# Performance work log

Measured on AMD Instinct MI355X. Metric: run time of the kernel, lower is better.

Reference implementation:

```python
import jax, jax.numpy as jnp
import numpy as np

N = 12288   # nodes
E = 393216  # edges (avg degree 32)
B = 16      # graphs in batch
F_IN = 15   # node feature dim
H = 32      # hidden_dim
EMB = 64    # embedding_dim
NC = 11     # num_classes
EDIM = 2    # edge feature dim
EPS = 1e-5  # BatchNorm eps


def _bn(x, gamma, beta):
    # training-mode BatchNorm1d: biased batch variance, matches torch normalization
    mu = jnp.mean(x, axis=0)
    var = jnp.var(x, axis=0)
    return gamma * (x - mu) * jax.lax.rsqrt(var + EPS) + beta


def setup_inputs() -> dict:
    key = jax.random.key(0)
    ks = jax.random.split(key, 16)
    def p(k, shape, s=0.05):
        return jax.random.normal(k, shape, dtype=jnp.float32) * s
    z = lambda *s: jnp.zeros(s, jnp.float32)
    o = lambda *s: jnp.ones(s, jnp.float32)
    return {
        "x": jax.random.normal(ks[0], (N, F_IN), dtype=jnp.float32),
        "edge_attr": jax.random.normal(ks[1], (E, EDIM), dtype=jnp.float32),
        "w_edge": p(ks[2], (EDIM, 1)), "b_edge": z(1),
        "w1": p(ks[3], (F_IN, H)), "b1": z(H), "g1": o(H), "be1": z(H),
        "w2": p(ks[4], (H, 2 * H)), "b2": z(2 * H), "g2": o(2 * H), "be2": z(2 * H),
        "w3": p(ks[5], (2 * H, EMB)), "b3": z(EMB), "g3": o(EMB), "be3": z(EMB),
        "wf1": p(ks[6], (EMB, 512)), "bf1": z(512), "gf1": o(512), "bef1": z(512),
        "wf2": p(ks[7], (512, 256)), "bf2": z(256), "gf2": o(256), "bef2": z(256),
        "wf3": p(ks[8], (256, NC)), "bf3": z(NC),
        "edge_index": jax.random.randint(ks[9], (2, E), 0, N, dtype=jnp.int64)
                      if jax.config.jax_enable_x64 else jax.random.randint(ks[9], (2, E), 0, N),
        "batch": jnp.sort(jax.random.randint(ks[10], (N,), 0, B)),
    }


def reference(x, edge_attr, w_edge, b_edge,
              w1, b1, g1, be1, w2, b2, g2, be2, w3, b3, g3, be3,
              wf1, bf1, gf1, bef1, wf2, bf2, gf2, bef2, wf3, bf3,
              edge_index, batch):
    # edge weights: sigmoid(Linear(edge_attr)) -> [E]
    ew = jax.nn.sigmoid(edge_attr @ w_edge + b_edge)[:, 0]
    # dense adjacency with self loops, accumulate duplicates (sparse_coo.to_dense)
    loop = jnp.arange(N)
    row = jnp.concatenate([edge_index[0], loop])
    col = jnp.concatenate([edge_index[1], loop])
    w_aug = jnp.concatenate([ew, jnp.ones((N,), ew.dtype)])
    adj = jnp.zeros((N, N), ew.dtype).at[row, col].add(w_aug)
    # symmetric degree normalization D^-1/2 A D^-1/2
    deg = adj.sum(axis=1)
    dis = jnp.where(deg > 0, jax.lax.rsqrt(jnp.where(deg > 0, deg, 1.0)), 0.0)
    support = dis[:, None] * adj * dis[None, :]
    # three GCN layers: support @ x @ W + b, BN, relu
    h = jax.nn.relu(_bn(support @ x @ w1 + b1, g1, be1))
    h = jax.nn.relu(_bn(support @ h @ w2 + b2, g2, be2))
    h = jax.nn.relu(_bn(support @ h @ w3 + b3, g3, be3))
    # global max pool per graph (empty graphs -> zeros)
    seg = jax.ops.segment_max(h, batch, num_segments=B)
    cnt = jax.ops.segment_sum(jnp.ones((N,), h.dtype), batch, num_segments=B)
    emb = jnp.where(cnt[:, None] > 0, seg, 0.0)
    # MLP head (dropout = identity at inference)
    o = jax.nn.relu(_bn(emb @ wf1 + bf1, gf1, bef1))
    o = jax.nn.relu(_bn(o @ wf2 + bf2, gf2, bef2))
    logits = o @ wf3 + bf3
    return jax.nn.log_softmax(logits, axis=1), emb
```

## Files before the change

kernel.cpp:

```cpp
#include <hip/hip_runtime.h>
#include <hip/hip_bf16.h>

#define NN   12288
#define EE   393216
#define WELL 128
#define NELL (NN*WELL)
#define BG   16
#define FIN  15
#define FH1  32
#define FH2  64
#define NCL  11
#define BNEPS 1e-5f
#define NBANK 32

typedef unsigned long long u64;
static inline int cdiv(long a, long b){ return (int)((a + b - 1) / b); }

__device__ __forceinline__ int getIdx(const void* p, long i, int is64){
  return is64 ? (int)((const long long*)p)[i] : ((const int*)p)[i];
}

__device__ __forceinline__ float degOf(unsigned lo){
  return 1.0f + (float)lo * (1.0f/1048576.0f);
}

__global__ void k_pre(u64* deg_cnt, float* csp1, float* csp2, float* csp3,
                      float* embf, const void* ei, const void* batch, int* flags){
  int g = blockIdx.x*256 + threadIdx.x;
  if (g < NN) deg_cnt[g] = 0ull;
  if (g < NBANK*128){ csp1[g] = 0.f; csp2[g] = 0.f; csp3[g] = 0.f; }
  if (g < BG*64) embf[g] = 0.f;
  if (blockIdx.x == 0 && threadIdx.x < 64){
    const int* a = (const int*)ei;
    unsigned long long m0 = __ballot(a[2*threadIdx.x + 1] == 0);
    const int* b = (const int*)batch;
    int j = 96*threadIdx.x;
    unsigned long long m1 = __ballot(b[2*j + 1] == 0);
    if (threadIdx.x == 0){
      flags[0] = (m0 == ~0ull) ? 1 : 0;
      flags[1] = (m1 == ~0ull) ? 1 : 0;
    }
  }
}

__global__ void k_edge(const float* ea, const float* we, const float* bedg,
                       const void* ei, const int* flags, u64* deg_cnt, u64* csr_p){
  int e = blockIdx.x*256 + threadIdx.x;
  if (e >= EE) return;
  int is64 = flags[0];
  float2 eav = ((const float2*)ea)[e];
  float z = eav.x*we[0] + eav.y*we[1] + bedg[0];
  float w = 1.0f/(1.0f + expf(-z));
  int r = getIdx(ei, e, is64);
  int c = getIdx(ei, (long)EE + e, is64);
  u64 add = (1ull << 32) | (u64)__float2uint_rn(w * 1048576.0f);
  u64 old = atomicAdd(&deg_cnt[r], add);
  int slot = (int)(old >> 32);
  if (slot < WELL)
    csr_p[((long)r << 7) + slot] = (u64)(unsigned)c | ((u64)__float_as_uint(w) << 32);
}

template<int F, int FP, int FO, int APPLY_BN>
__global__ void __launch_bounds__(256) k_layer(
    const float* __restrict__ Hin,
    const float* __restrict__ cspin, const float* __restrict__ gam,
    const float* __restrict__ bet,
    const float* __restrict__ W, const float* __restrict__ bias,
    const u64* __restrict__ deg_cnt, const u64* __restrict__ csr_p,
    float* __restrict__ Pout, float* __restrict__ csout){
  const int R = 256/FP;
  __shared__ float At[R][FP];
  __shared__ float lcs[FO], lcq[FO];
  __shared__ float lsc[64], lsh[64];
  if (threadIdx.x < FO){ lcs[threadIdx.x] = 0.f; lcq[threadIdx.x] = 0.f; }
  if (APPLY_BN && threadIdx.x < F){
    float s = 0.f, q = 0.f;
    #pragma unroll
    for (int b = 0; b < NBANK; b++){
      s += cspin[b*128 + threadIdx.x];
      q += cspin[b*128 + 64 + threadIdx.x];
    }
    float mu  = s*(1.0f/NN);
    float var = q*(1.0f/NN) - mu*mu;
    float sc = gam[threadIdx.x]*rsqrtf(var + BNEPS);
    lsc[threadIdx.x] = sc;
    lsh[threadIdx.x] = bet[threadIdx.x] - mu*sc;
  }
  __syncthreads();
  int f = threadIdx.x % FP, lr = threadIdx.x / FP;
  float sc = 1.f, sh = 0.f;
  if (APPLY_BN && f < F){ sc = lsc[f]; sh = lsh[f]; }
  int row = blockIdx.x*R + lr;
  const unsigned* __restrict__ cl = (const unsigned*)deg_cnt;
  if (f < F){
    u64 dc = deg_cnt[row];
    float d = rsqrtf(degOf((unsigned)(dc & 0xffffffffull)));
    int n = (int)(dc >> 32);
    n = n < WELL ? n : WELL;
    float v0 = Hin[row*F + f];
    if (APPLY_BN) v0 = fmaxf(v0*sc + sh, 0.f);
    float acc = d * v0;
    int nch = (n + 15) >> 4;
    const uint4* pb = (const uint4*)(csr_p + ((long)row << 7));
    if (nch > 0){
      uint4 a[8], b[8];
      #pragma unroll
      for (int j = 0; j < 8; j++) a[j] = pb[j];
      for (int ch = 0; ch < nch; ch++){
        bool more = (ch + 1 < nch);
        if (more){
          #pragma unroll
          for (int j = 0; j < 8; j++) b[j] = pb[8*ch + 8 + j];
        }
        int base = ch*16;
        if (base + 16 > n){
          #pragma unroll
          for (int j = 0; j < 8; j++){
            if (base + 2*j     >= n){ a[j].x = 0u; a[j].y = 0u; }
            if (base + 2*j + 1 >= n){ a[j].z = 0u; a[j].w = 0u; }
          }
        }
        #pragma unroll
        for (int j = 0; j < 8; j++){
          int c0 = (int)a[j].x, c1 = (int)a[j].z;
          float w0 = __uint_as_float(a[j].y) * rsqrtf(degOf(cl[2*c0]));
          float w1 = __uint_as_float(a[j].w) * rsqrtf(degOf(cl[2*c1]));
          float h0 = Hin[c0*F + f];
          float h1 = Hin[c1*F + f];
          if (APPLY_BN){
            h0 = fmaxf(h0*sc + sh, 0.f);
            h1 = fmaxf(h1*sc + sh, 0.f);
          }
          acc += w0*h0 + w1*h1;
        }
        if (more){
          #pragma unroll
          for (int j = 0; j < 8; j++) a[j] = b[j];
        }
      }
    }
    At[lr][f] = d * acc;
  }
  __syncthreads();
  const int fo = threadIdx.x % FO;
  float bb = bias[fo];
  for (int o = threadIdx.x; o < R*FO; o += 256){
    int l = o / FO;
    float s = bb;
    #pragma unroll
    for (int fi = 0; fi < F; fi++) s += At[l][fi] * W[fi*FO + fo];
    Pout[(blockIdx.x*R + l)*FO + fo] = s;
    atomicAdd(&lcs[fo], s);
    atomicAdd(&lcq[fo], s*s);
  }
  __syncthreads();
  if (threadIdx.x < FO){
    int bank = blockIdx.x & (NBANK-1);
    atomicAdd(&csout[bank*128 + threadIdx.x],      lcs[threadIdx.x]);
    atomicAdd(&csout[bank*128 + 64 + threadIdx.x], lcq[threadIdx.x]);
  }
}

__global__ void k_pool(const float* P3, const float* csp, const float* gam,
                       const float* bet, const void* batch, const int* flags,
                       float* embf){
  __shared__ float lsc[64], lsh[64];
  if (threadIdx.x < 64){
    float s = 0.f, q = 0.f;
    #pragma unroll
    for (int b = 0; b < NBANK; b++){
      s += csp[b*128 + threadIdx.x];
      q += csp[b*128 + 64 + threadIdx.x];
    }
    float mu  = s*(1.0f/NN);
    float var = q*(1.0f/NN) - mu*mu;
    float sc = gam[threadIdx.x]*rsqrtf(var + BNEPS);
    lsc[threadIdx.x] = sc;
    lsh[threadIdx.x] = bet[threadIdx.x] - mu*sc;
  }
  __syncthreads();
  int is64 = flags[1];
  int b = blockIdx.x & 15, chunk = blockIdx.x >> 4;
  int lo = 0, hi = NN;
  while (lo < hi){ int m = (lo+hi)>>1; if (getIdx(batch, m, is64) < b) lo = m+1; else hi = m; }
  int start = lo;
  lo = start; hi = NN;
  while (lo < hi){ int m = (lo+hi)>>1; if (getIdx(batch, m, is64) < b+1) lo = m+1; else hi = m; }
  int end = lo;
  int f = threadIdx.x & 63, grp = threadIdx.x >> 6;
  float sc = lsc[f], sh = lsh[f];
  float m = 0.0f;
  for (int i = start + chunk*4 + grp; i < end; i += 64)
    m = fmaxf(m, P3[(long)i*FH2 + f]*sc + sh);
  __shared__ float shm[4][64];
  shm[grp][f] = m;
  __syncthreads();
  if (grp == 0){
    float v = fmaxf(fmaxf(shm[0][f], shm[1][f]), fmaxf(shm[2][f], shm[3][f]));
    atomicMax((int*)&embf[b*64 + f], __float_as_int(v));
  }
}

__global__ void __launch_bounds__(256) k_fcA(const float* embf, const float* wf1,
    const float* bf1, const float* gf1, const float* bef1, float* s1g, float* out){
  if (blockIdx.x == 0){
    #pragma unroll
    for (int i = 0; i < 4; i++)
      out[BG*NCL + i*256 + threadIdx.x] = embf[i*256 + threadIdx.x];
  }
  int c = blockIdx.x*4 + (threadIdx.x >> 6);
  int l = threadIdx.x & 63;
  float wcol = wf1[l*512 + c];
  float z[BG];
  #pragma unroll
  for (int r = 0; r < BG; r++){
    float v = embf[r*64 + l] * wcol;
    #pragma unroll
    for (int off = 32; off > 0; off >>= 1) v += __shfl_down(v, off);
    z[r] = v;
  }
  if (l == 0){
    float bb = bf1[c];
    float s = 0.f, q = 0.f;
    #pragma unroll
    for (int r = 0; r < BG; r++){ float zr = z[r] + bb; s += zr; q += zr*zr; }
    float mean = s*(1.f/BG), var = q*(1.f/BG) - mean*mean;
    float inv = rsqrtf(var + BNEPS);
    float gg = gf1[c], b2 = bef1[c];
    #pragma unroll
    for (int r = 0; r < BG; r++)
      s1g[r*512 + c] = fmaxf(gg*(z[r] + bb - mean)*inv + b2, 0.f);
  }
}

__global__ void __launch_bounds__(256) k_fcB(const float* s1g, const float* wf2,
    const float* bf2, const float* gf2, const float* bef2, float* s2g){
  int c = blockIdx.x*4 + (threadIdx.x >> 6);
  int l = threadIdx.x & 63;
  float wreg[8];
  #pragma unroll
  for (int j = 0; j < 8; j++) wreg[j] = wf2[(l + 64*j)*256 + c];
  float z[BG];
  #pragma unroll
  for (int r = 0; r < BG; r++){
    float v = 0.f;
    #pragma unroll
    for (int j = 0; j < 8; j++) v += s1g[r*512 + l + 64*j] * wreg[j];
    #pragma unroll
    for (int off = 32; off > 0; off >>= 1) v += __shfl_down(v, off);
    z[r] = v;
  }
  if (l == 0){
    float bb = bf2[c];
    float s = 0.f, q = 0.f;
    #pragma unroll
    for (int r = 0; r < BG; r++){ float zr = z[r] + bb; s += zr; q += zr*zr; }
    float mean = s*(1.f/BG), var = q*(1.f/BG) - mean*mean;
    float inv = rsqrtf(var + BNEPS);
    float gg = gf2[c], b2 = bef2[c];
    #pragma unroll
    for (int r = 0; r < BG; r++)
      s2g[r*256 + c] = fmaxf(gg*(z[r] + bb - mean)*inv + b2, 0.f);
  }
}

__global__ void k_fc3(const float* s2g, const float* wf3, const float* bf3, float* out){
  __shared__ float s2[BG*256];
  __shared__ float sl[BG*NCL];
  int t = threadIdx.x;
  for (int i = t; i < BG*256; i += 256) s2[i] = s2g[i];
  __syncthreads();
  if (t < BG*NCL){
    int r = t / NCL, c = t - r*NCL;
    float s = bf3[c];
    for (int k = 0; k < 256; k++) s += s2[r*256 + k]*wf3[k*NCL + c];
    sl[t] = s;
  }
  __syncthreads();
  if (t < BG){
    float m = -1e30f;
    for (int c = 0; c < NCL; c++) m = fmaxf(m, sl[t*NCL + c]);
    float s = 0.f;
    for (int c = 0; c < NCL; c++) s += expf(sl[t*NCL + c] - m);
    float lg = logf(s) + m;
    for (int c = 0; c < NCL; c++) out[t*NCL + c] = sl[t*NCL + c] - lg;
  }
}

extern "C" void kernel_launch(void* const* d_in, const int* in_sizes, int n_in,
                              void* d_out, int out_size, void* d_ws, size_t ws_size,
                              hipStream_t stream){
  const float* x    = (const float*)d_in[0];
  const float* ea   = (const float*)d_in[1];
  const float* we   = (const float*)d_in[2];
  const float* bedg = (const float*)d_in[3];
  const float* w1   = (const float*)d_in[4];  const float* b1  = (const float*)d_in[5];
  const float* g1   = (const float*)d_in[6];  const float* be1 = (const float*)d_in[7];
  const float* w2   = (const float*)d_in[8];  const float* b2  = (const float*)d_in[9];
  const float* g2   = (const float*)d_in[10]; const float* be2 = (const float*)d_in[11];
  const float* w3   = (const float*)d_in[12]; const float* b3  = (const float*)d_in[13];
  const float* g3   = (const float*)d_in[14]; const float* be3 = (const float*)d_in[15];
  const float* wf1  = (const float*)d_in[16]; const float* bf1 = (const float*)d_in[17];
  const float* gf1  = (const float*)d_in[18]; const float* bef1= (const float*)d_in[19];
  const float* wf2  = (const float*)d_in[20]; const float* bf2 = (const float*)d_in[21];
  const float* gf2  = (const float*)d_in[22]; const float* bef2= (const float*)d_in[23];
  const float* wf3  = (const float*)d_in[24]; const float* bf3 = (const float*)d_in[25];
  const void* ei    = d_in[26];
  const void* batch = d_in[27];
  float* out = (float*)d_out;

  u64* wq = (u64*)d_ws;
  u64* deg_cnt = wq; wq += NN;
  u64* csr_p   = wq; wq += NELL;
  float* ws = (float*)wq;
  float* P1    = ws; ws += NN*FH1;
  float* P2    = ws; ws += NN*FH2;
  float* P3    = ws; ws += NN*FH2;
  float* csp1  = ws; ws += NBANK*128;
  float* csp2  = ws; ws += NBANK*128;
  float* csp3  = ws; ws += NBANK*128;
  float* embf  = ws; ws += BG*64;
  float* s1g   = ws; ws += BG*512;
  float* s2g   = ws; ws += BG*256;
  int* flags   = (int*)ws;

  k_pre<<<48, 256, 0, stream>>>(deg_cnt, csp1, csp2, csp3, embf, ei, batch, flags);
  k_edge<<<cdiv(EE,256), 256, 0, stream>>>(ea, we, bedg, ei, flags, deg_cnt, csr_p);

  k_layer<FIN,16,FH1,0><<<NN/16, 256, 0, stream>>>(x, nullptr, nullptr, nullptr,
      w1, b1, deg_cnt, csr_p, P1, csp1);
  k_layer<FH1,32,FH2,1><<<NN/8, 256, 0, stream>>>(P1, csp1, g1, be1,
      w2, b2, deg_cnt, csr_p, P2, csp2);
  k_layer<FH2,64,FH2,1><<<NN/4, 256, 0, stream>>>(P2, csp2, g2, be2,
      w3, b3, deg_cnt, csr_p, P3, csp3);

  k_pool<<<256, 256, 0, stream>>>(P3, csp3, g3, be3, batch, flags, embf);
  k_fcA<<<128, 256, 0, stream>>>(embf, wf1, bf1, gf1, bef1, s1g, out);
  k_fcB<<<64, 256, 0, stream>>>(s1g, wf2, bf2, gf2, bef2, s2g);
  k_fc3<<<1, 256, 0, stream>>>(s2g, wf3, bf3, out);
}
```

Baseline: 238.0 us.

## Pack CSR entries into 32-bit fixed-point and prefold column degree normalization

Each CSR entry shrinks from 64 bits (column index plus float weight) to 32 bits: a 14-bit column index and an 18-bit fixed-point weight. A new pass after edge construction multiplies every edge weight by the column's inverse square-root degree, so the three layer kernels no longer gather the degree array per edge. The layer loop now issues all 16 feature gathers before accumulating, which exposes more memory-level parallelism. The cost is an extra kernel launch and reduced weight precision (about 1/131072 quantization), which could affect agreement with the reference.

```diff
diff --git a/kernel.cpp b/kernel.cpp
--- a/kernel.cpp
+++ b/kernel.cpp
@@ -44,7 +44,8 @@
 }
 
 __global__ void k_edge(const float* ea, const float* we, const float* bedg,
-                       const void* ei, const int* flags, u64* deg_cnt, u64* csr_p){
+                       const void* ei, const int* flags, u64* deg_cnt,
+                       unsigned* csr_p){
   int e = blockIdx.x*256 + threadIdx.x;
   if (e >= EE) return;
   int is64 = flags[0];
@@ -56,8 +57,27 @@
   u64 add = (1ull << 32) | (u64)__float2uint_rn(w * 1048576.0f);
   u64 old = atomicAdd(&deg_cnt[r], add);
   int slot = (int)(old >> 32);
-  if (slot < WELL)
-    csr_p[((long)r << 7) + slot] = (u64)(unsigned)c | ((u64)__float_as_uint(w) << 32);
+  if (slot < WELL){
+    unsigned wfix = __float2uint_rn(w * 131072.0f);
+    csr_p[((long)r << 7) + slot] = (unsigned)c | (wfix << 14);
+  }
+}
+
+__global__ void __launch_bounds__(256) k_fix2(const u64* __restrict__ deg_cnt,
+                                              unsigned* __restrict__ csr_p){
+  int row = blockIdx.x*4 + (threadIdx.x >> 6);
+  int lane = threadIdx.x & 63;
+  const unsigned* cl = (const unsigned*)deg_cnt;
+  int n = (int)(deg_cnt[row] >> 32);
+  n = n < WELL ? n : WELL;
+  for (int s = lane; s < n; s += 64){
+    long idx = ((long)row << 7) + s;
+    unsigned v = csr_p[idx];
+    int c = (int)(v & 16383u);
+    float w = (float)(v >> 14) * (1.0f/131072.0f);
+    w *= rsqrtf(degOf(cl[2*c]));
+    csr_p[idx] = (unsigned)c | (__float2uint_rn(w * 131072.0f) << 14);
+  }
 }
 
 template<int F, int FP, int FO, int APPLY_BN>
@@ -66,7 +86,7 @@
     const float* __restrict__ cspin, const float* __restrict__ gam,
     const float* __restrict__ bet,
     const float* __restrict__ W, const float* __restrict__ bias,
-    const u64* __restrict__ deg_cnt, const u64* __restrict__ csr_p,
+    const u64* __restrict__ deg_cnt, const unsigned* __restrict__ csr_p,
     float* __restrict__ Pout, float* __restrict__ csout){
   const int R = 256/FP;
   __shared__ float At[R][FP];
@@ -91,7 +111,6 @@
   float sc = 1.f, sh = 0.f;
   if (APPLY_BN && f < F){ sc = lsc[f]; sh = lsh[f]; }
   int row = blockIdx.x*R + lr;
-  const unsigned* __restrict__ cl = (const unsigned*)deg_cnt;
   if (f < F){
     u64 dc = deg_cnt[row];
     float d = rsqrtf(degOf((unsigned)(dc & 0xffffffffull)));
@@ -103,39 +122,38 @@
     int nch = (n + 15) >> 4;
     const uint4* pb = (const uint4*)(csr_p + ((long)row << 7));
     if (nch > 0){
-      uint4 a[8], b[8];
+      uint4 a[4], b[4];
       #pragma unroll
-      for (int j = 0; j < 8; j++) a[j] = pb[j];
+      for (int j = 0; j < 4; j++) a[j] = pb[j];
       for (int ch = 0; ch < nch; ch++){
         bool more = (ch + 1 < nch);
         if (more){
           #pragma unroll
-          for (int j = 0; j < 8; j++) b[j] = pb[8*ch + 8 + j];
+          for (int j = 0; j < 4; j++) b[j] = pb[4*ch + 4 + j];
         }
+        unsigned pv[16];
+        pv[0]=a[0].x; pv[1]=a[0].y; pv[2]=a[0].z; pv[3]=a[0].w;
+        pv[4]=a[1].x; pv[5]=a[1].y; pv[6]=a[1].z; pv[7]=a[1].w;
+        pv[8]=a[2].x; pv[9]=a[2].y; pv[10]=a[2].z; pv[11]=a[2].w;
+        pv[12]=a[3].x; pv[13]=a[3].y; pv[14]=a[3].z; pv[15]=a[3].w;
         int base = ch*16;
         if (base + 16 > n){
           #pragma unroll
-          for (int j = 0; j < 8; j++){
-            if (base + 2*j     >= n){ a[j].x = 0u; a[j].y = 0u; }
-            if (base + 2*j + 1 >= n){ a[j].z = 0u; a[j].w = 0u; }
-          }
+          for (int j = 0; j < 16; j++) if (base + j >= n) pv[j] = 0u;
         }
+        float hh[16];
         #pragma unroll
-        for (int j = 0; j < 8; j++){
-          int c0 = (int)a[j].x, c1 = (int)a[j].z;
-          float w0 = __uint_as_float(a[j].y) * rsqrtf(degOf(cl[2*c0]));
-          float w1 = __uint_as_float(a[j].w) * rsqrtf(degOf(cl[2*c1]));
-          float h0 = Hin[c0*F + f];
-          float h1 = Hin[c1*F + f];
-          if (APPLY_BN){
-            h0 = fmaxf(h0*sc + sh, 0.f);
-            h1 = fmaxf(h1*sc + sh, 0.f);
-          }
-          acc += w0*h0 + w1*h1;
+        for (int j = 0; j < 16; j++)
+          hh[j] = Hin[(int)(pv[j] & 16383u)*F + f];
+        #pragma unroll
+        for (int j = 0; j < 16; j++){
+          float h = hh[j];
+          if (APPLY_BN) h = fmaxf(h*sc + sh, 0.f);
+          acc += (float)(pv[j] >> 14) * (1.0f/131072.0f) * h;
         }
         if (more){
           #pragma unroll
-          for (int j = 0; j < 8; j++) a[j] = b[j];
+          for (int j = 0; j < 4; j++) a[j] = b[j];
         }
       }
     }
@@ -311,7 +329,7 @@
 
   u64* wq = (u64*)d_ws;
   u64* deg_cnt = wq; wq += NN;
-  u64* csr_p   = wq; wq += NELL;
+  unsigned* csr_p = (unsigned*)wq; wq += NELL/2;
   float* ws = (float*)wq;
   float* P1    = ws; ws += NN*FH1;
   float* P2    = ws; ws += NN*FH2;
@@ -326,6 +344,7 @@
 
   k_pre<<<48, 256, 0, stream>>>(deg_cnt, csp1, csp2, csp3, embf, ei, batch, flags);
   k_edge<<<cdiv(EE,256), 256, 0, stream>>>(ea, we, bedg, ei, flags, deg_cnt, csr_p);
+  k_fix2<<<NN/4, 256, 0, stream>>>(deg_cnt, csr_p);
 
   k_layer<FIN,16,FH1,0><<<NN/16, 256, 0, stream>>>(x, nullptr, nullptr, nullptr,
       w1, b1, deg_cnt, csr_p, P1, csp1);
```

After: 228.7 us. 1.04x faster.
